# Kernel optimization log

Hardware: AMD Instinct MI355X
Metric: run time of the kernel (lower is better)

## Reference

```python
import jax, jax.numpy as jnp
import numpy as np
from jax import lax

RF, NLF, MESH, FUSION = 64, 16, 16, 64


def _conv3x3(x, w, b):
    # stride 1, pad 1, ksize 3 == SAME
    y = lax.conv_general_dilated(x, w, (1, 1), 'SAME',
                                 dimension_numbers=('NCHW', 'OIHW', 'NCHW'))
    return y + b[None, :, None, None]


def _bn(x, g, b, m, v, eps=1e-5):
    scale = g / jnp.sqrt(v + eps)
    return (x - m[None, :, None, None]) * scale[None, :, None, None] + b[None, :, None, None]


def _rct_block(x, w1, b1, g, be, m, v, w2, b2):
    # extra_conv=True: Conv -> BN -> SiLU -> Conv (all stride 1)
    h = jax.nn.silu(_bn(_conv3x3(x, w1, b1), g, be, m, v))
    return _conv3x3(h, w2, b2)


def setup_inputs():
    key = jax.random.key(0)
    ks = jax.random.split(key, 8)
    B, H, W = 4, 512, 512
    return {
        'feature': jax.random.normal(ks[0], (B, RF, H, W), jnp.float32),
        'p_low': jax.random.normal(ks[1], (B, FUSION, MESH + 1, MESH + 1), jnp.float32),
        'r_w1': jax.random.normal(ks[2], (FUSION, FUSION, 3, 3), jnp.float32) * 0.05,
        'r_b1': jnp.zeros((FUSION,), jnp.float32),
        'r_gamma': jnp.ones((FUSION,), jnp.float32),
        'r_beta': jnp.zeros((FUSION,), jnp.float32),
        'r_mean': jnp.zeros((FUSION,), jnp.float32),
        'r_var': jnp.ones((FUSION,), jnp.float32),
        'r_w2': jax.random.normal(ks[3], (RF * NLF, FUSION, 3, 3), jnp.float32) * 0.05,
        'r_b2': jnp.zeros((RF * NLF,), jnp.float32),
        't_w1': jax.random.normal(ks[4], (FUSION, FUSION, 3, 3), jnp.float32) * 0.05,
        't_b1': jnp.zeros((FUSION,), jnp.float32),
        't_gamma': jnp.ones((FUSION,), jnp.float32),
        't_beta': jnp.zeros((FUSION,), jnp.float32),
        't_mean': jnp.zeros((FUSION,), jnp.float32),
        't_var': jnp.ones((FUSION,), jnp.float32),
        't_w2': jax.random.normal(ks[5], (3 * NLF, FUSION, 3, 3), jnp.float32) * 0.05,
        't_b2': jnp.zeros((3 * NLF,), jnp.float32),
    }


def reference(feature, p_low, r_w1, r_b1, r_gamma, r_beta, r_mean, r_var, r_w2, r_b2,
              t_w1, t_b1, t_gamma, t_beta, t_mean, t_var, t_w2, t_b2):
    B, C, H, W = feature.shape
    M = MESH
    mh, mw = H // M, W // M  # H,W divisible by mesh_size -> pad_tensor is identity
    P = mh * mw

    r_l = _rct_block(p_low, r_w1, r_b1, r_gamma, r_beta, r_mean, r_var, r_w2, r_b2)  # [B, RF*NLF, M+1, M+1]
    t_l = _rct_block(p_low, t_w1, t_b1, t_gamma, t_beta, t_mean, t_var, t_w2, t_b2)  # [B, 3*NLF, M+1, M+1]

    # channel dim factors as (feat, nlf); corners concat along nlf axis in order
    # (i,j), (i,j+1), (i+1,j), (i+1,j+1) -> K = 4*NLF keys per tile
    rc = r_l.reshape(B, RF, NLF, M + 1, M + 1)
    rk = jnp.concatenate([rc[..., :M, :M], rc[..., :M, 1:],
                          rc[..., 1:, :M], rc[..., 1:, 1:]], axis=2)  # [B,RF,4NLF,M,M]
    tc = t_l.reshape(B, 3, NLF, M + 1, M + 1)
    tk = jnp.concatenate([tc[..., :M, :M], tc[..., :M, 1:],
                          tc[..., 1:, :M], tc[..., 1:, 1:]], axis=2)  # [B,3,4NLF,M,M]

    # split feature into tiles: [B, M, M, P, RF] (row-major pixel order within tile)
    f = feature.reshape(B, RF, M, mh, M, mw).transpose(0, 2, 4, 3, 5, 1).reshape(B, M, M, P, RF)

    scale = 1.0 / jnp.sqrt(jnp.float32(RF))
    att = jnp.einsum('bxypr,brkxy->bxypk', f, rk) * scale  # [B,M,M,P,4NLF]
    att = jax.nn.softmax(att, axis=-1)
    out = jnp.einsum('bxypk,bckxy->bxycp', att, tk)  # [B,M,M,3,P]

    Y = out.reshape(B, M, M, 3, mh, mw).transpose(0, 3, 1, 4, 2, 5).reshape(B, 3, H, W)
    return Y
```

## Files before the change

kernel.cpp:

```cpp
#include <hip/hip_runtime.h>

typedef unsigned short u16;
typedef __bf16 bf16x8 __attribute__((ext_vector_type(8)));
typedef unsigned short us8 __attribute__((ext_vector_type(8)));
typedef float f32x4 __attribute__((ext_vector_type(4)));
typedef unsigned int u32x4 __attribute__((ext_vector_type(4)));

union U8u { us8 s; u16 u[8]; };

__device__ __forceinline__ u16 f2bf(float f){
  unsigned u = __builtin_bit_cast(unsigned, f);
  u += 0x7fffu + ((u >> 16) & 1u);
  return (u16)(u >> 16);
}
__device__ __forceinline__ bf16x8 asbf(us8 x){ return __builtin_bit_cast(bf16x8, x); }

#define MFMA16(a,b,c) __builtin_amdgcn_mfma_f32_16x16x32_bf16((a),(b),(c),0,0,0)

__device__ __forceinline__ void stage_zero2(u16* sS, int tid){
  uint* z = (uint*)sS;
  for (int i = tid; i < 12996; i += 256) z[i] = 0u;
}

__device__ __forceinline__ void stage_src_f32T(const float* __restrict__ src,
                                               u16* sS, int tid){
  for (int i4 = tid; i4 < 4624; i4 += 256){
    int e = i4 * 4;
    f32x4 dv = *(const f32x4*)(src + e);
    #pragma unroll
    for (int t = 0; t < 4; t++){
      int ee = e + t;
      int ci = ee / 289; int rr = ee - ci*289;
      int oy = rr / 17;  int ox = rr - oy*17;
      sS[((oy+1)*19 + ox+1)*72 + ci] = f2bf(dv[t]);
    }
  }
}

__device__ __forceinline__ void stage_src_bf16T(const u16* __restrict__ src,
                                                u16* sS, int tid){
  for (int i8 = tid; i8 < 2312; i8 += 256){
    int e = i8 * 8;
    U8u dv; dv.s = *(const us8*)(src + e);
    #pragma unroll
    for (int t = 0; t < 8; t++){
      int ee = e + t;
      int ci = ee / 289; int rr = ee - ci*289;
      int oy = rr / 17;  int ox = rr - oy*17;
      sS[((oy+1)*19 + ox+1)*72 + ci] = dv.u[t];
    }
  }
}

__device__ __forceinline__ void stage_w_f32(const float* __restrict__ w, int m0,
                                            u16* sW, int tid){
  for (int i4 = tid; i4 < 2304; i4 += 256){
    int e = i4 * 4;
    int co = e / 576; int r0 = e - co*576;
    f32x4 wv = *(const f32x4*)(w + (size_t)(m0+co)*576 + r0);
    #pragma unroll
    for (int t = 0; t < 4; t++){
      int r = r0 + t; int cin = r / 9; int tap = r - cin*9;
      sW[co*584 + tap*64 + cin] = f2bf(wv[t]);
    }
  }
}

__device__ __forceinline__ f32x4 conv_tile2(const u16* sS, const u16* sW,
                                            int nt, int l15, int q)
{
  int p = nt*16 + l15; int pc = p > 288 ? 288 : p;
  int oy = pc / 17, ox = pc - oy*17;
  f32x4 acc = {0.f, 0.f, 0.f, 0.f};
  #pragma unroll
  for (int ks = 0; ks < 18; ks++){
    const int tap = ks >> 1;
    const int dy = tap / 3, dx = tap - dy*3;
    int pix2 = (oy+dy)*19 + (ox+dx);
    us8 bv = *(const us8*)(sS + pix2*72 + (ks & 1)*32 + q*8);
    us8 av = *(const us8*)(sW + l15*584 + ks*32 + q*8);
    acc = MFMA16(asbf(av), asbf(bv), acc);
  }
  return acc;
}

__global__ __launch_bounds__(256) void conv1_k(
    const float* __restrict__ p_low,
    const float* __restrict__ wR, const float* __restrict__ b1R,
    const float* __restrict__ gR, const float* __restrict__ beR,
    const float* __restrict__ mR, const float* __restrict__ vR,
    const float* __restrict__ wT, const float* __restrict__ b1T,
    const float* __restrict__ gT, const float* __restrict__ beT,
    const float* __restrict__ mT, const float* __restrict__ vT,
    u16* __restrict__ hR, u16* __restrict__ hT)
{
  __shared__ __attribute__((aligned(16))) u16 sS[25992];
  __shared__ __attribute__((aligned(16))) u16 sW[9344];
  int tid = threadIdx.x;
  int bx = blockIdx.x;
  int job = bx >> 6;
  int b = (bx >> 4) & 3;
  int m0 = ((bx >> 2) & 3) << 4;
  int px = bx & 3;
  int nt0 = px * 5, ntEnd = nt0 + 5 > 19 ? 19 : nt0 + 5;
  const float* w  = job ? wT  : wR;
  const float* b1 = job ? b1T : b1R;
  const float* g  = job ? gT  : gR;
  const float* be = job ? beT : beR;
  const float* mn = job ? mT  : mR;
  const float* vr = job ? vT  : vR;
  u16* out = job ? hT : hR;
  const float* src = p_low + (size_t)b * 18496;

  stage_zero2(sS, tid);
  __syncthreads();
  stage_src_f32T(src, sS, tid);
  stage_w_f32(w, m0, sW, tid);
  __syncthreads();

  int lane = tid & 63, wave = tid >> 6;
  int l15 = lane & 15, q = lane >> 4;
  float scl[4], sft[4];
  #pragma unroll
  for (int e = 0; e < 4; e++){
    int co = m0 + q*4 + e;
    float s = g[co] / sqrtf(vr[co] + 1e-5f);
    scl[e] = s;
    sft[e] = (b1[co] - mn[co]) * s + be[co];
  }
  for (int nt = nt0 + wave; nt < ntEnd; nt += 4){
    f32x4 acc = conv_tile2(sS, sW, nt, l15, q);
    int p = nt*16 + l15;
    if (p < 289){
      #pragma unroll
      for (int e = 0; e < 4; e++){
        float y = acc[e]*scl[e] + sft[e];
        float si = y / (1.f + __expf(-y));
        out[(size_t)(b*64 + m0 + q*4 + e)*289 + p] = f2bf(si);
      }
    }
  }
}

__global__ __launch_bounds__(256) void conv2_k(
    const u16* __restrict__ hR, const u16* __restrict__ hT,
    const float* __restrict__ w2R, const float* __restrict__ b2R,
    const float* __restrict__ w2T, const float* __restrict__ b2T,
    u16* __restrict__ rlq, float* __restrict__ tlq)
{
  __shared__ __attribute__((aligned(16))) u16 sS[25992];
  __shared__ __attribute__((aligned(16))) u16 sW[9344];
  int tid = threadIdx.x;
  int bx = blockIdx.x;
  const float *w, *bias; const u16* src;
  int b, m0, px, isR;
  if (bx < 512){
    isR = 1; b = bx >> 7; int rem = bx & 127;
    m0 = (rem >> 1) << 4; px = rem & 1;
    src = hR + (size_t)b*18496; w = w2R; bias = b2R;
  } else {
    isR = 0; int i = bx - 512; b = i / 6; int rr = i - b*6;
    m0 = (rr >> 1) << 4; px = rr & 1;
    src = hT + (size_t)b*18496; w = w2T; bias = b2T;
  }
  int nt0 = px * 10, ntEnd = px ? 19 : 10;

  stage_zero2(sS, tid);
  __syncthreads();
  stage_src_bf16T(src, sS, tid);
  stage_w_f32(w, m0, sW, tid);
  __syncthreads();

  int lane = tid & 63, wave = tid >> 6;
  int l15 = lane & 15, q = lane >> 4;
  float bs[4];
  #pragma unroll
  for (int e = 0; e < 4; e++) bs[e] = bias[m0 + q*4 + e];
  for (int nt = nt0 + wave; nt < ntEnd; nt += 4){
    f32x4 acc = conv_tile2(sS, sW, nt, l15, q);
    int p = nt*16 + l15;
    if (p < 289){
      if (isR){
        uint2 pk;
        pk.x = (uint)f2bf((acc[0]+bs[0])*0.125f)
             | ((uint)f2bf((acc[1]+bs[1])*0.125f) << 16);
        pk.y = (uint)f2bf((acc[2]+bs[2])*0.125f)
             | ((uint)f2bf((acc[3]+bs[3])*0.125f) << 16);
        *(uint2*)(rlq + ((size_t)b*289 + p)*1024 + m0 + q*4) = pk;
      } else {
        f32x4 ov = {acc[0]+bs[0], acc[1]+bs[1], acc[2]+bs[2], acc[3]+bs[3]};
        *(f32x4*)(tlq + ((size_t)b*289 + p)*48 + m0 + q*4) = ov;
      }
    }
  }
}

__global__ __launch_bounds__(256) void attn_k(
    const uint* __restrict__ feat,
    const u16* __restrict__ rlq, const float* __restrict__ tlq,
    float* __restrict__ out)
{
  __shared__ __attribute__((aligned(16))) u16 rkT[4608];
  __shared__ float tkF[256];
  int tid = threadIdx.x;
  int ty = blockIdx.x, tx = blockIdx.y, b = blockIdx.z;
  int lane = tid & 63, wave = tid >> 6;
  int l15 = lane & 15, q = lane >> 4;

  {
    int corner = wave;
    int pix = (tx + (corner >> 1))*17 + ty + (corner & 1);
    const u16* sp = rlq + ((size_t)b*289 + pix)*1024 + lane*16;
    U8u v0, v1; v0.s = *(const us8*)sp; v1.s = *(const us8*)(sp + 8);
    #pragma unroll
    for (int nl = 0; nl < 8; nl++){
      rkT[(corner*16 + nl)*72 + lane]     = v0.u[nl];
      rkT[(corner*16 + 8 + nl)*72 + lane] = v1.u[nl];
    }
  }
  if (tid < 192){
    int corner = tid / 48; int idx = tid - corner*48;
    int pix = (tx + (corner >> 1))*17 + ty + (corner & 1);
    int c = idx >> 4, nl = idx & 15;
    tkF[c*64 + corner*16 + nl] = tlq[((size_t)b*289 + pix)*48 + idx];
  } else {
    tkF[192 + (tid - 192)] = 1.f;
  }
  __syncthreads();

  bf16x8 frk[4][2];
  #pragma unroll
  for (int nt = 0; nt < 4; nt++)
    #pragma unroll
    for (int ks = 0; ks < 2; ks++)
      frk[nt][ks] = __builtin_bit_cast(bf16x8,
          *(const us8*)(rkT + (nt*16 + l15)*72 + ks*32 + q*8));

  float tkr[4][4];
  #pragma unroll
  for (int c = 0; c < 4; c++)
    #pragma unroll
    for (int nt = 0; nt < 4; nt++)
      tkr[c][nt] = tkF[c*64 + nt*16 + l15];

  const size_t HW = (size_t)512*512;
  for (int cnk = 0; cnk < 16; cnk++){
    int irow = (wave << 3) + (cnk >> 1);
    int j0 = (cnk & 1) << 4;
    int hh = tx*32 + irow;
    const uint* fb = feat + ((size_t)b*64 + q*8)*HW + (size_t)hh*512
                          + (ty*32 + j0 + l15);
    uint r0[8], r1[8];
    #pragma unroll
    for (int j = 0; j < 8; j++){
      r0[j] = fb[(size_t)j*HW];
      r1[j] = fb[(size_t)(j+32)*HW];
    }
    u32x4 p0, p1;
    #pragma unroll
    for (int j2 = 0; j2 < 4; j2++){
      p0[j2] = __builtin_amdgcn_perm(r0[2*j2+1], r0[2*j2], 0x07060302u);
      p1[j2] = __builtin_amdgcn_perm(r1[2*j2+1], r1[2*j2], 0x07060302u);
    }
    bf16x8 A0 = __builtin_bit_cast(bf16x8, p0);
    bf16x8 A1 = __builtin_bit_cast(bf16x8, p1);

    f32x4 acc[4];
    #pragma unroll
    for (int nt = 0; nt < 4; nt++){
      f32x4 zz = {0.f, 0.f, 0.f, 0.f};
      zz = MFMA16(A0, frk[nt][0], zz);
      zz = MFMA16(A1, frk[nt][1], zz);
      acc[nt] = zz;
    }
    #pragma unroll
    for (int nt = 0; nt < 4; nt++)
      #pragma unroll
      for (int e = 0; e < 4; e++)
        acc[nt][e] = __expf(acc[nt][e]);
    float o[4][4];
    #pragma unroll
    for (int c = 0; c < 4; c++)
      #pragma unroll
      for (int e = 0; e < 4; e++)
        o[c][e] = acc[0][e]*tkr[c][0] + acc[1][e]*tkr[c][1]
                + acc[2][e]*tkr[c][2] + acc[3][e]*tkr[c][3];
    #pragma unroll
    for (int mask = 1; mask < 16; mask <<= 1)
      #pragma unroll
      for (int c = 0; c < 4; c++)
        #pragma unroll
        for (int e = 0; e < 4; e++)
          o[c][e] += __shfl_xor(o[c][e], mask, 64);
    if (l15 < 3){
      float i0 = __builtin_amdgcn_rcpf(o[3][0]);
      float i1 = __builtin_amdgcn_rcpf(o[3][1]);
      float i2 = __builtin_amdgcn_rcpf(o[3][2]);
      float i3 = __builtin_amdgcn_rcpf(o[3][3]);
      f32x4 ov;
      ov[0] = o[l15][0]*i0; ov[1] = o[l15][1]*i1;
      ov[2] = o[l15][2]*i2; ov[3] = o[l15][3]*i3;
      *(f32x4*)(out + ((size_t)(b*3 + l15)*512 + hh)*512
                    + (ty*32 + j0 + q*4)) = ov;
    }
  }
}

extern "C" void kernel_launch(void* const* d_in, const int* in_sizes, int n_in,
                              void* d_out, int out_size, void* d_ws, size_t ws_size,
                              hipStream_t stream)
{
  (void)in_sizes; (void)n_in; (void)out_size; (void)ws_size;
  const uint*  feature = (const uint*)d_in[0];
  const float* p_low = (const float*)d_in[1];
  const float* r_w1 = (const float*)d_in[2];
  const float* r_b1 = (const float*)d_in[3];
  const float* r_g  = (const float*)d_in[4];
  const float* r_be = (const float*)d_in[5];
  const float* r_m  = (const float*)d_in[6];
  const float* r_v  = (const float*)d_in[7];
  const float* r_w2 = (const float*)d_in[8];
  const float* r_b2 = (const float*)d_in[9];
  const float* t_w1 = (const float*)d_in[10];
  const float* t_b1 = (const float*)d_in[11];
  const float* t_g  = (const float*)d_in[12];
  const float* t_be = (const float*)d_in[13];
  const float* t_m  = (const float*)d_in[14];
  const float* t_v  = (const float*)d_in[15];
  const float* t_w2 = (const float*)d_in[16];
  const float* t_b2 = (const float*)d_in[17];

  char* ws = (char*)d_ws;
  u16* hR = (u16*)ws;
  u16* hT = hR + (size_t)4*64*289;
  u16* rlq = (u16*)(ws + 295936);
  float* tlq = (float*)(ws + 295936 + 2367488);
  float* outp = (float*)d_out;

  hipLaunchKernelGGL(conv1_k, dim3(128), dim3(256), 0, stream,
      p_low, r_w1, r_b1, r_g, r_be, r_m, r_v,
      t_w1, t_b1, t_g, t_be, t_m, t_v, hR, hT);
  hipLaunchKernelGGL(conv2_k, dim3(536), dim3(256), 0, stream,
      hR, hT, r_w2, r_b2, t_w2, t_b2, rlq, tlq);
  hipLaunchKernelGGL(attn_k, dim3(16, 16, 4), dim3(256), 0, stream,
      feature, rlq, tlq, outp);
}
```

Baseline: 470.5 us.

## Transpose attention MFMA so keys land per-lane, cutting shuffle reductions

The operand order of the score MFMA is swapped so each lane holds scores for one pixel across keys instead of one key across pixels. This replaces a 16-lane butterfly of 64 shuffles per chunk with 8 cross-quad shuffles. The value weights are now loaded as vector registers, and the softmax scale is folded with log2(e) into the stored keys so the raw exp2 instruction can be used. Output stores become scalar per-lane writes by three quads instead of f32x4 stores, which may reduce store coalescing.

Measured after the change: 456.9 us. -2.9%, faster.

```diff
diff --git a/kernel.cpp b/kernel.cpp
--- a/kernel.cpp
+++ b/kernel.cpp
@@ -176,16 +176,17 @@
   float bs[4];
   #pragma unroll
   for (int e = 0; e < 4; e++) bs[e] = bias[m0 + q*4 + e];
+  const float PSC = 0.18033688f;
   for (int nt = nt0 + wave; nt < ntEnd; nt += 4){
     f32x4 acc = conv_tile2(sS, sW, nt, l15, q);
     int p = nt*16 + l15;
     if (p < 289){
       if (isR){
         uint2 pk;
-        pk.x = (uint)f2bf((acc[0]+bs[0])*0.125f)
-             | ((uint)f2bf((acc[1]+bs[1])*0.125f) << 16);
-        pk.y = (uint)f2bf((acc[2]+bs[2])*0.125f)
-             | ((uint)f2bf((acc[3]+bs[3])*0.125f) << 16);
+        pk.x = (uint)f2bf((acc[0]+bs[0])*PSC)
+             | ((uint)f2bf((acc[1]+bs[1])*PSC) << 16);
+        pk.y = (uint)f2bf((acc[2]+bs[2])*PSC)
+             | ((uint)f2bf((acc[3]+bs[3])*PSC) << 16);
         *(uint2*)(rlq + ((size_t)b*289 + p)*1024 + m0 + q*4) = pk;
       } else {
         f32x4 ov = {acc[0]+bs[0], acc[1]+bs[1], acc[2]+bs[2], acc[3]+bs[3]};
@@ -201,7 +202,7 @@
     float* __restrict__ out)
 {
   __shared__ __attribute__((aligned(16))) u16 rkT[4608];
-  __shared__ float tkF[256];
+  __shared__ __attribute__((aligned(16))) float tkF[256];
   int tid = threadIdx.x;
   int ty = blockIdx.x, tx = blockIdx.y, b = blockIdx.z;
   int lane = tid & 63, wave = tid >> 6;
@@ -236,12 +237,12 @@
       frk[nt][ks] = __builtin_bit_cast(bf16x8,
           *(const us8*)(rkT + (nt*16 + l15)*72 + ks*32 + q*8));
 
-  float tkr[4][4];
-  #pragma unroll
-  for (int c = 0; c < 4; c++)
+  f32x4 tkc[3][4];
+  #pragma unroll
+  for (int c = 0; c < 3; c++)
     #pragma unroll
     for (int nt = 0; nt < 4; nt++)
-      tkr[c][nt] = tkF[c*64 + nt*16 + l15];
+      tkc[c][nt] = *(const f32x4*)(tkF + c*64 + nt*16 + q*4);
 
   const size_t HW = (size_t)512*512;
   for (int cnk = 0; cnk < 16; cnk++){
@@ -269,40 +270,33 @@
     #pragma unroll
     for (int nt = 0; nt < 4; nt++){
       f32x4 zz = {0.f, 0.f, 0.f, 0.f};
-      zz = MFMA16(A0, frk[nt][0], zz);
-      zz = MFMA16(A1, frk[nt][1], zz);
+      zz = MFMA16(frk[nt][0], A0, zz);
+      zz = MFMA16(frk[nt][1], A1, zz);
       acc[nt] = zz;
     }
+    float den = 0.f, o0 = 0.f, o1 = 0.f, o2 = 0.f;
     #pragma unroll
     for (int nt = 0; nt < 4; nt++)
       #pragma unroll
-      for (int e = 0; e < 4; e++)
-        acc[nt][e] = __expf(acc[nt][e]);
-    float o[4][4];
-    #pragma unroll
-    for (int c = 0; c < 4; c++)
-      #pragma unroll
-      for (int e = 0; e < 4; e++)
-        o[c][e] = acc[0][e]*tkr[c][0] + acc[1][e]*tkr[c][1]
-                + acc[2][e]*tkr[c][2] + acc[3][e]*tkr[c][3];
-    #pragma unroll
-    for (int mask = 1; mask < 16; mask <<= 1)
-      #pragma unroll
-      for (int c = 0; c < 4; c++)
-        #pragma unroll
-        for (int e = 0; e < 4; e++)
-          o[c][e] += __shfl_xor(o[c][e], mask, 64);
-    if (l15 < 3){
-      float i0 = __builtin_amdgcn_rcpf(o[3][0]);
-      float i1 = __builtin_amdgcn_rcpf(o[3][1]);
-      float i2 = __builtin_amdgcn_rcpf(o[3][2]);
-      float i3 = __builtin_amdgcn_rcpf(o[3][3]);
-      f32x4 ov;
-      ov[0] = o[l15][0]*i0; ov[1] = o[l15][1]*i1;
-      ov[2] = o[l15][2]*i2; ov[3] = o[l15][3]*i3;
-      *(f32x4*)(out + ((size_t)(b*3 + l15)*512 + hh)*512
-                    + (ty*32 + j0 + q*4)) = ov;
-    }
+      for (int e = 0; e < 4; e++){
+        float p = __builtin_amdgcn_exp2f(acc[nt][e]);
+        den += p;
+        o0 = fmaf(p, tkc[0][nt][e], o0);
+        o1 = fmaf(p, tkc[1][nt][e], o1);
+        o2 = fmaf(p, tkc[2][nt][e], o2);
+      }
+    o0  += __shfl_xor(o0, 16, 64);
+    o1  += __shfl_xor(o1, 16, 64);
+    o2  += __shfl_xor(o2, 16, 64);
+    den += __shfl_xor(den, 16, 64);
+    o0  += __shfl_xor(o0, 32, 64);
+    o1  += __shfl_xor(o1, 32, 64);
+    o2  += __shfl_xor(o2, 32, 64);
+    den += __shfl_xor(den, 32, 64);
+    float rin = __builtin_amdgcn_rcpf(den);
+    float val = (q == 0) ? o0 : ((q == 1) ? o1 : o2);
+    if (q < 3)
+      out[((size_t)(b*3 + q)*512 + hh)*512 + (ty*32 + j0 + l15)] = val * rin;
   }
 }
 
```
